# Kernel optimization log

Measured on AMD Instinct MI355X. Metric: run time of the kernel, lower is better.

## Reference

```python
import jax, jax.numpy as jnp
import numpy as np

S, H, R, Z, P = 268, 1024, 8, 8, 4
A = S - Z - P          # actual_hidden_dim = 256
E = min(Z, P)          # min_embed_dim = 4
B = 8192


def setup_inputs() -> dict:
    key = jax.random.key(0)
    ks = jax.random.split(key, 16)
    def g(k, shape, scale=0.02):
        return jax.random.normal(k, shape, dtype=jnp.float32) * scale
    return dict(
        t=jax.random.uniform(ks[0], (1,), dtype=jnp.float32) * 24.0,
        state=jax.random.normal(ks[1], (B, S), dtype=jnp.float32),
        W0=g(ks[2], (H, S + 2)), b0=jnp.zeros((H,), jnp.float32),
        res_W1=g(ks[3], (R, H, H)), res_b1=jnp.zeros((R, H), jnp.float32),
        res_W2=g(ks[4], (R, H, H)), res_b2=jnp.zeros((R, H), jnp.float32),
        Wf=g(ks[5], (S, H)), bf=jnp.zeros((S,), jnp.float32),
        lp_in_w=g(ks[6], (3 * E, E)), lp_in_b=jnp.zeros((3 * E,), jnp.float32),
        lp_out_w=g(ks[7], (E, E)), lp_out_b=jnp.zeros((E,), jnp.float32),
        ta_in_w=g(ks[8], (3 * A, A)), ta_in_b=jnp.zeros((3 * A,), jnp.float32),
        ta_out_w=g(ks[9], (A, A)), ta_out_b=jnp.zeros((A,), jnp.float32),
        loc_proj_w=g(ks[10], (E, Z)), loc_proj_b=jnp.zeros((E,), jnp.float32),
        loc_back_w=g(ks[11], (Z, E)), loc_back_b=jnp.zeros((Z,), jnp.float32),
    )


def reference(t, state, W0, b0, res_W1, res_b1, res_W2, res_b2, Wf, bf,
              lp_in_w, lp_in_b, lp_out_w, lp_out_b,
              ta_in_w, ta_in_b, ta_out_w, ta_out_b,
              loc_proj_w, loc_proj_b, loc_back_w, loc_back_b):
    Bn = state.shape[0]
    # time features: [sin(2*pi*t/24), cos(2*pi*t/24)] broadcast to [B, 2]
    ang = t * (2.0 * jnp.pi / 24.0)
    t_vec = jnp.broadcast_to(jnp.concatenate([jnp.sin(ang), jnp.cos(ang)]), (Bn, 2))

    # core MLP trunk: Linear -> ReLU -> R residual blocks -> Linear
    x = jnp.concatenate([state, t_vec], axis=-1)
    h = jax.nn.relu(x @ W0.T + b0)

    def block(h, p):
        W1, b1, W2, b2 = p
        return jnp.tanh(h + jnp.tanh(h @ W1.T + b1) @ W2.T + b2), None

    h, _ = jax.lax.scan(block, h, (res_W1, res_b1, res_W2, res_b2))
    core = h @ Wf.T + bf  # [B, S]

    # Attention deltas. Both MHA calls have key/value seq_len == 1, so the
    # softmax over a single key is exactly 1.0 and the output reduces exactly
    # to out_proj(v_proj(value)); Q/K projections (and the padded time query)
    # cancel mathematically. Same math as nn.MultiheadAttention here.
    h_part = state[:, :A]
    loc = state[:, A:A + Z]
    loc_p = loc @ loc_proj_w.T + loc_proj_b                   # [B, E]
    v = loc_p @ lp_in_w[2 * E:].T + lp_in_b[2 * E:]           # V projection
    enhanced_loc = v @ lp_out_w.T + lp_out_b                  # out projection
    delta_loc = (enhanced_loc - loc_p) @ loc_back_w.T + loc_back_b  # [B, Z]

    v2 = h_part @ ta_in_w[2 * A:].T + ta_in_b[2 * A:]
    enhanced_h = v2 @ ta_out_w.T + ta_out_b
    delta_h = enhanced_h - h_part                             # [B, A]

    delta = jnp.concatenate(
        [delta_h, delta_loc, jnp.zeros((Bn, P), state.dtype)], axis=-1)
    return core + 0.1 * delta
```

## Files before the change

### kernel.cpp

```cpp
#include <hip/hip_runtime.h>
#include <hip/hip_bf16.h>


typedef unsigned short u16;
typedef __bf16 bf16x8 __attribute__((ext_vector_type(8)));
typedef float f32x4 __attribute__((ext_vector_type(4)));

__device__ __forceinline__ u16 f2b(float f) {
  union { float f; unsigned u; } v; v.f = f;
  unsigned r = v.u + 0x7FFFu + ((v.u >> 16) & 1u);
  return (u16)(r >> 16);
}
__device__ __forceinline__ float b2f(u16 s) {
  union { unsigned u; float f; } v; v.u = ((unsigned)s) << 16;
  return v.f;
}

__device__ __forceinline__ void g2l16(const u16* g, u16* l) {
  __builtin_amdgcn_global_load_lds(
      (__attribute__((address_space(1))) void*)g,
      (__attribute__((address_space(3))) void*)l, 16, 0, 0);
}

template<int MODE, int KK, int LDA>
__global__ __launch_bounds__(512, 2)
void pgemm(const u16* __restrict__ A, const u16* __restrict__ W,
           const float* __restrict__ bias, const u16* __restrict__ resid,
           void* __restrict__ outp, int nreal, int ldo)
{
  extern __shared__ __align__(16) u16 sm[];
  u16* Asb = sm;
  u16* Bsb = sm + 2 * 256 * 64;

  const int tid  = threadIdx.x;
  const int wave = tid >> 6;
  const int lane = tid & 63;
  const int m0 = blockIdx.x << 8;
  const int n0 = blockIdx.y << 7;
  const int wr = wave >> 1, wc = wave & 1;
  const int lrow = lane & 15, quad = lane >> 4;
  const int sw = lrow & 7;

  const int srow  = lane >> 3;
  const int sperm = ((lane & 7) ^ (srow & 7)) << 3;

  const u16* Ag = A + (size_t)(m0 + wave * 32 + srow) * LDA + sperm;
  const u16* Bg = W + (size_t)(n0 + wave * 16 + srow) * KK + sperm;

  f32x4 acc[4][4];
#pragma unroll
  for (int i = 0; i < 4; i++)
#pragma unroll
    for (int j = 0; j < 4; j++) { f32x4 z = {0.f,0.f,0.f,0.f}; acc[i][j] = z; }

#pragma unroll
  for (int g = 0; g < 4; g++)
    g2l16(Ag + (size_t)g * 8 * LDA, Asb + (wave * 32 + g * 8) * 64);
#pragma unroll
  for (int g = 0; g < 2; g++)
    g2l16(Bg + (size_t)g * 8 * KK, Bsb + (wave * 16 + g * 8) * 64);
  __syncthreads();

  const int P = KK / 64;
  for (int p = 0; p < P; p++) {
    if (p + 1 < P) {
      const int ko = (p + 1) << 6;
      const int bo = ((p + 1) & 1);
      u16* aD = Asb + bo * 256 * 64;
      u16* bD = Bsb + bo * 128 * 64;
#pragma unroll
      for (int g = 0; g < 4; g++)
        g2l16(Ag + (size_t)g * 8 * LDA + ko, aD + (wave * 32 + g * 8) * 64);
#pragma unroll
      for (int g = 0; g < 2; g++)
        g2l16(Bg + (size_t)g * 8 * KK + ko, bD + (wave * 16 + g * 8) * 64);
    }
    const u16* aS = Asb + (p & 1) * 256 * 64;
    const u16* bS = Bsb + (p & 1) * 128 * 64;
#pragma unroll
    for (int s = 0; s < 2; s++) {
      const int phys = (s * 4 + quad) ^ sw;
      bf16x8 af[4], bfr[4];
#pragma unroll
      for (int i = 0; i < 4; i++)
        af[i] = *(const bf16x8*)&aS[(wr * 64 + i * 16 + lrow) * 64 + phys * 8];
#pragma unroll
      for (int j = 0; j < 4; j++)
        bfr[j] = *(const bf16x8*)&bS[(wc * 64 + j * 16 + lrow) * 64 + phys * 8];
#pragma unroll
      for (int i = 0; i < 4; i++)
#pragma unroll
        for (int j = 0; j < 4; j++)
          acc[i][j] = __builtin_amdgcn_mfma_f32_16x16x32_bf16(af[i], bfr[j], acc[i][j], 0, 0, 0);
    }
    __syncthreads();
  }

  auto th = [](float x) {
    x = fminf(fmaxf(x, -40.f), 40.f);
    float a = __builtin_amdgcn_exp2f(2.88539008177793f * x);
    return (a - 1.f) * __builtin_amdgcn_rcpf(a + 1.f);
  };

#pragma unroll
  for (int i = 0; i < 4; i++) {
    const int rowb = m0 + wr * 64 + i * 16 + quad * 4;
#pragma unroll
    for (int j = 0; j < 4; j++) {
      const int col = n0 + wc * 64 + j * 16 + lrow;
      const float bi = (col < nreal) ? bias[col] : 0.f;
#pragma unroll
      for (int r = 0; r < 4; r++) {
        const int row = rowb + r;
        float v = acc[i][j][r] + bi;
        if (MODE == 0) {
          v = v > 0.f ? v : 0.f;
          ((u16*)outp)[(size_t)row * ldo + col] = f2b(v);
        } else if (MODE == 1) {
          ((u16*)outp)[(size_t)row * ldo + col] = f2b(th(v));
        } else if (MODE == 2) {
          v += b2f(resid[(size_t)row * ldo + col]);
          ((u16*)outp)[(size_t)row * ldo + col] = f2b(th(v));
        } else if (MODE == 3) {
          if (col < nreal) ((float*)outp)[(size_t)row * ldo + col] = v;
        }
      }
    }
  }
}

__global__ __launch_bounds__(256, 4)
void gemm_bt(const u16* __restrict__ A, const u16* __restrict__ B,
             const float* __restrict__ bias, u16* __restrict__ outp,
             int K, int lda, int ldo)
{
  __shared__ __align__(16) u16 As[64 * 64];
  __shared__ __align__(16) u16 Bs[128 * 64];
  const int tid  = threadIdx.x;
  const int wave = tid >> 6;
  const int lane = tid & 63;
  const int m0 = blockIdx.y << 6;
  const int n0 = blockIdx.x << 7;
  const int wr = wave >> 1, wc = wave & 1;
  const int lrow = lane & 15, quad = lane >> 4;
  const int srow  = lane >> 3;
  const int sperm = ((lane & 7) ^ (srow & 7)) << 3;

  const u16* Ag0 = A + (size_t)(m0 + wave * 16 +  0 + srow) * lda + sperm;
  const u16* Ag1 = A + (size_t)(m0 + wave * 16 +  8 + srow) * lda + sperm;
  const u16* Bg0 = B + (size_t)(n0 + wave * 32 +  0 + srow) * K + sperm;
  const u16* Bg1 = B + (size_t)(n0 + wave * 32 +  8 + srow) * K + sperm;
  const u16* Bg2 = B + (size_t)(n0 + wave * 32 + 16 + srow) * K + sperm;
  const u16* Bg3 = B + (size_t)(n0 + wave * 32 + 24 + srow) * K + sperm;
  u16* Al0 = &As[(wave * 16 +  0) * 64];
  u16* Al1 = &As[(wave * 16 +  8) * 64];
  u16* Bl0 = &Bs[(wave * 32 +  0) * 64];
  u16* Bl1 = &Bs[(wave * 32 +  8) * 64];
  u16* Bl2 = &Bs[(wave * 32 + 16) * 64];
  u16* Bl3 = &Bs[(wave * 32 + 24) * 64];

  f32x4 acc[2][4];
#pragma unroll
  for (int i = 0; i < 2; i++)
#pragma unroll
    for (int j = 0; j < 4; j++) { f32x4 z = {0.f,0.f,0.f,0.f}; acc[i][j] = z; }

  const int swz = lrow & 7;

  for (int k0 = 0; k0 < K; k0 += 64) {
    if (k0) __syncthreads();
    g2l16(Ag0 + k0, Al0);
    g2l16(Ag1 + k0, Al1);
    g2l16(Bg0 + k0, Bl0);
    g2l16(Bg1 + k0, Bl1);
    g2l16(Bg2 + k0, Bl2);
    g2l16(Bg3 + k0, Bl3);
    __syncthreads();
#pragma unroll
    for (int s = 0; s < 2; s++) {
      const int c = (s * 4 + quad) ^ swz;
      bf16x8 af[2], bfr[4];
#pragma unroll
      for (int i = 0; i < 2; i++)
        af[i] = *(const bf16x8*)&As[(wr * 32 + i * 16 + lrow) * 64 + c * 8];
#pragma unroll
      for (int j = 0; j < 4; j++)
        bfr[j] = *(const bf16x8*)&Bs[(wc * 64 + j * 16 + lrow) * 64 + c * 8];
#pragma unroll
      for (int i = 0; i < 2; i++)
#pragma unroll
        for (int j = 0; j < 4; j++)
          acc[i][j] = __builtin_amdgcn_mfma_f32_16x16x32_bf16(af[i], bfr[j], acc[i][j], 0, 0, 0);
    }
  }

#pragma unroll
  for (int i = 0; i < 2; i++) {
    const int rowb = m0 + wr * 32 + i * 16 + quad * 4;
#pragma unroll
    for (int j = 0; j < 4; j++) {
      const int col = n0 + wc * 64 + j * 16 + lrow;
      const float bi = bias[col];
#pragma unroll
      for (int r = 0; r < 4; r++)
        outp[(size_t)(rowb + r) * ldo + col] = f2b(acc[i][j][r] + bi);
    }
  }
}

__global__ void conv_bulk(const float* __restrict__ w1, const float* __restrict__ w2,
                          u16* __restrict__ o1, u16* __restrict__ o2)
{
  const int n4 = (8 * 1024 * 1024) / 4;
  int i = blockIdx.x * 256 + threadIdx.x;
  const float* src; u16* dst;
  if (i < n4) { src = w1; dst = o1; }
  else        { i -= n4; if (i >= n4) return; src = w2; dst = o2; }
  float4 v = ((const float4*)src)[i];
  unsigned p0 = (unsigned)f2b(v.x) | ((unsigned)f2b(v.y) << 16);
  unsigned p1 = (unsigned)f2b(v.z) | ((unsigned)f2b(v.w) << 16);
  uint2 pk; pk.x = p0; pk.y = p1;
  ((uint2*)dst)[i] = pk;
}

__global__ void conv_misc(const float* __restrict__ W0, const float* __restrict__ Wf,
                          const float* __restrict__ ta_in_w, const float* __restrict__ ta_out_w,
                          const float* __restrict__ state, const float* __restrict__ t,
                          u16* __restrict__ w0_bf, u16* __restrict__ wf_bf,
                          u16* __restrict__ taA, u16* __restrict__ taB,
                          u16* __restrict__ x_bf)
{
  int i = blockIdx.x * 256 + threadIdx.x;
  const int nW0 = 1024 * 384;
  const int nWf = 384 * 1024;
  const int nTa = 256 * 256;
  const int nX  = 8192 * 384;
  if (i < nW0) {
    int o = i / 384, k = i - o * 384;
    w0_bf[i] = (k < 270) ? f2b(W0[o * 270 + k]) : (u16)0;
    return;
  }
  i -= nW0;
  if (i < nWf) {
    int n = i >> 10;
    wf_bf[i] = (n < 268) ? f2b(Wf[i]) : (u16)0;
    return;
  }
  i -= nWf;
  if (i < nTa) { taA[i] = f2b(ta_in_w[512 * 256 + i]); return; }
  i -= nTa;
  if (i < nTa) { taB[i] = f2b(ta_out_w[i]); return; }
  i -= nTa;
  if (i < nX) {
    int r = i / 384, c = i - r * 384;
    u16 v;
    if (c < 268) v = f2b(state[r * 268 + c]);
    else if (c == 268) { float ang = t[0] * 0.2617993877991494f; v = f2b(sinf(ang)); }
    else if (c == 269) { float ang = t[0] * 0.2617993877991494f; v = f2b(cosf(ang)); }
    else v = 0;
    x_bf[i] = v;
  }
}

__global__ void add_delta(float* __restrict__ out, const u16* __restrict__ eh,
                          const float* __restrict__ state,
                          const float* __restrict__ lp_in_w, const float* __restrict__ lp_in_b,
                          const float* __restrict__ lp_out_w, const float* __restrict__ lp_out_b,
                          const float* __restrict__ loc_proj_w, const float* __restrict__ loc_proj_b,
                          const float* __restrict__ loc_back_w, const float* __restrict__ loc_back_b)
{
  const int idx = blockIdx.x * 256 + threadIdx.x;
  if (idx >= 8192 * 268) return;
  const int row = idx / 268;
  const int col = idx - row * 268;
  if (col < 256) {
    out[idx] += 0.1f * (b2f(eh[row * 256 + col]) - state[idx]);
  } else if (col < 264) {
    const float* srow = state + row * 268 + 256;
    float locp[4], vv[4], dd[4];
#pragma unroll
    for (int e = 0; e < 4; e++) {
      float s = loc_proj_b[e];
#pragma unroll
      for (int z = 0; z < 8; z++) s += loc_proj_w[e * 8 + z] * srow[z];
      locp[e] = s;
    }
#pragma unroll
    for (int e = 0; e < 4; e++) {
      float s = lp_in_b[8 + e];
#pragma unroll
      for (int j = 0; j < 4; j++) s += lp_in_w[(8 + e) * 4 + j] * locp[j];
      vv[e] = s;
    }
#pragma unroll
    for (int e = 0; e < 4; e++) {
      float s = lp_out_b[e];
#pragma unroll
      for (int j = 0; j < 4; j++) s += lp_out_w[e * 4 + j] * vv[j];
      dd[e] = s - locp[e];
    }
    const int z = col - 256;
    float s = loc_back_b[z];
#pragma unroll
    for (int e = 0; e < 4; e++) s += loc_back_w[z * 4 + e] * dd[e];
    out[idx] += 0.1f * s;
  }
}

extern "C" void kernel_launch(void* const* d_in, const int* in_sizes, int n_in,
                              void* d_out, int out_size, void* d_ws, size_t ws_size,
                              hipStream_t stream)
{
  const float* t          = (const float*)d_in[0];
  const float* state      = (const float*)d_in[1];
  const float* W0         = (const float*)d_in[2];
  const float* b0         = (const float*)d_in[3];
  const float* rW1        = (const float*)d_in[4];
  const float* rb1        = (const float*)d_in[5];
  const float* rW2        = (const float*)d_in[6];
  const float* rb2        = (const float*)d_in[7];
  const float* Wf         = (const float*)d_in[8];
  const float* bfv        = (const float*)d_in[9];
  const float* lp_in_w    = (const float*)d_in[10];
  const float* lp_in_b    = (const float*)d_in[11];
  const float* lp_out_w   = (const float*)d_in[12];
  const float* lp_out_b   = (const float*)d_in[13];
  const float* ta_in_w    = (const float*)d_in[14];
  const float* ta_in_b    = (const float*)d_in[15];
  const float* ta_out_w   = (const float*)d_in[16];
  const float* ta_out_b   = (const float*)d_in[17];
  const float* loc_proj_w = (const float*)d_in[18];
  const float* loc_proj_b = (const float*)d_in[19];
  const float* loc_back_w = (const float*)d_in[20];
  const float* loc_back_b = (const float*)d_in[21];
  float* out = (float*)d_out;

  char* ws = (char*)d_ws;
  auto alloc = [&](size_t bytes) { char* p = ws; ws += (bytes + 255) & ~(size_t)255; return p; };
  u16* rw1_bf = (u16*)alloc((size_t)8 * 1024 * 1024 * 2);
  u16* rw2_bf = (u16*)alloc((size_t)8 * 1024 * 1024 * 2);
  u16* w0_bf  = (u16*)alloc((size_t)1024 * 384 * 2);
  u16* wf_bf  = (u16*)alloc((size_t)384 * 1024 * 2);
  u16* taA_bf = (u16*)alloc((size_t)256 * 256 * 2);
  u16* taB_bf = (u16*)alloc((size_t)256 * 256 * 2);
  u16* x_bf   = (u16*)alloc((size_t)8192 * 384 * 2);
  u16* h_bf   = (u16*)alloc((size_t)8192 * 1024 * 2);
  u16* tmp_bf = (u16*)alloc((size_t)8192 * 1024 * 2);
  u16* v2_bf  = (u16*)alloc((size_t)8192 * 256 * 2);
  u16* eh_bf  = (u16*)alloc((size_t)8192 * 256 * 2);

  const int lds = (2 * 256 * 64 + 2 * 128 * 64) * 2;
  hipFuncSetAttribute(reinterpret_cast<const void*>(pgemm<0, 384, 384>),
                      hipFuncAttributeMaxDynamicSharedMemorySize, lds);
  hipFuncSetAttribute(reinterpret_cast<const void*>(pgemm<1, 1024, 1024>),
                      hipFuncAttributeMaxDynamicSharedMemorySize, lds);
  hipFuncSetAttribute(reinterpret_cast<const void*>(pgemm<2, 1024, 1024>),
                      hipFuncAttributeMaxDynamicSharedMemorySize, lds);
  hipFuncSetAttribute(reinterpret_cast<const void*>(pgemm<3, 1024, 1024>),
                      hipFuncAttributeMaxDynamicSharedMemorySize, lds);

  conv_bulk<<<16384, 256, 0, stream>>>(rW1, rW2, rw1_bf, rw2_bf);
  conv_misc<<<15872, 256, 0, stream>>>(W0, Wf, ta_in_w, ta_out_w, state, t,
                                       w0_bf, wf_bf, taA_bf, taB_bf, x_bf);

  pgemm<0, 384, 384><<<dim3(32, 8), 512, lds, stream>>>(x_bf, w0_bf, b0, nullptr, h_bf, 1024, 1024);

  for (int r = 0; r < 8; r++) {
    pgemm<1, 1024, 1024><<<dim3(32, 8), 512, lds, stream>>>(
        h_bf, rw1_bf + ((size_t)r << 20), rb1 + (r << 10), nullptr, tmp_bf, 1024, 1024);
    pgemm<2, 1024, 1024><<<dim3(32, 8), 512, lds, stream>>>(
        tmp_bf, rw2_bf + ((size_t)r << 20), rb2 + (r << 10), h_bf, h_bf, 1024, 1024);
  }

  gemm_bt<<<dim3(2, 128), 256, 0, stream>>>(x_bf, taA_bf, ta_in_b + 512, v2_bf, 256, 384, 256);
  gemm_bt<<<dim3(2, 128), 256, 0, stream>>>(v2_bf, taB_bf, ta_out_b, eh_bf, 256, 256, 256);

  pgemm<3, 1024, 1024><<<dim3(32, 3), 512, lds, stream>>>(h_bf, wf_bf, bfv, nullptr, out, 268, 268);

  add_delta<<<8576, 256, 0, stream>>>(out, eh_bf, state,
                                      lp_in_w, lp_in_b, lp_out_w, lp_out_b,
                                      loc_proj_w, loc_proj_b, loc_back_w, loc_back_b);
}
```

Before: 582.1 us.

## Triple-buffer GEMM LDS pipeline with vmcnt-based waits and MFMA priority

Replaces the two-stage LDS double buffer in the bf16 GEMM with a three-stage ring that prefetches two K-tiles ahead. The full __syncthreads per iteration becomes explicit vmcnt waits plus a raw s_barrier, and MFMA sections are wrapped in s_setprio. The goal is to hide global-to-LDS latency better. In exchange LDS per block grows from 96KB to 144KB, which likely cuts resident blocks per CU from two to one.

```diff
diff --git a/kernel.cpp b/kernel.cpp
--- a/kernel.cpp
+++ b/kernel.cpp
@@ -29,8 +29,7 @@
            void* __restrict__ outp, int nreal, int ldo)
 {
   extern __shared__ __align__(16) u16 sm[];
-  u16* Asb = sm;
-  u16* Bsb = sm + 2 * 256 * 64;
+  constexpr int BUFSZ = (256 + 128) * 64;
 
   const int tid  = threadIdx.x;
   const int wave = tid >> 6;
@@ -53,30 +52,34 @@
 #pragma unroll
     for (int j = 0; j < 4; j++) { f32x4 z = {0.f,0.f,0.f,0.f}; acc[i][j] = z; }
 
-#pragma unroll
-  for (int g = 0; g < 4; g++)
-    g2l16(Ag + (size_t)g * 8 * LDA, Asb + (wave * 32 + g * 8) * 64);
-#pragma unroll
-  for (int g = 0; g < 2; g++)
-    g2l16(Bg + (size_t)g * 8 * KK, Bsb + (wave * 16 + g * 8) * 64);
-  __syncthreads();
-
-  const int P = KK / 64;
-  for (int p = 0; p < P; p++) {
-    if (p + 1 < P) {
-      const int ko = (p + 1) << 6;
-      const int bo = ((p + 1) & 1);
-      u16* aD = Asb + bo * 256 * 64;
-      u16* bD = Bsb + bo * 128 * 64;
-#pragma unroll
-      for (int g = 0; g < 4; g++)
-        g2l16(Ag + (size_t)g * 8 * LDA + ko, aD + (wave * 32 + g * 8) * 64);
-#pragma unroll
-      for (int g = 0; g < 2; g++)
-        g2l16(Bg + (size_t)g * 8 * KK + ko, bD + (wave * 16 + g * 8) * 64);
-    }
-    const u16* aS = Asb + (p & 1) * 256 * 64;
-    const u16* bS = Bsb + (p & 1) * 128 * 64;
+  auto stage = [&](int p, int buf) {
+    const int ko = p << 6;
+    u16* aD = sm + buf * BUFSZ;
+    u16* bD = aD + 256 * 64;
+#pragma unroll
+    for (int g = 0; g < 4; g++)
+      g2l16(Ag + (size_t)g * 8 * LDA + ko, aD + (wave * 32 + g * 8) * 64);
+#pragma unroll
+    for (int g = 0; g < 2; g++)
+      g2l16(Bg + (size_t)g * 8 * KK + ko, bD + (wave * 16 + g * 8) * 64);
+  };
+
+  constexpr int P = KK / 64;
+
+  stage(0, 0);
+  stage(1, 1);
+  asm volatile("s_waitcnt vmcnt(6)" ::: "memory");
+  __builtin_amdgcn_s_barrier();
+  __builtin_amdgcn_sched_barrier(0);
+
+#pragma unroll
+  for (int p = 0; p < P; ++p) {
+    const int cur = p % 3;
+    const int stg = (p + 2) % 3;
+    if (p + 2 < P) stage(p + 2, stg);
+
+    const u16* aS = sm + cur * BUFSZ;
+    const u16* bS = aS + 256 * 64;
 #pragma unroll
     for (int s = 0; s < 2; s++) {
       const int phys = (s * 4 + quad) ^ sw;
@@ -87,13 +90,23 @@
 #pragma unroll
       for (int j = 0; j < 4; j++)
         bfr[j] = *(const bf16x8*)&bS[(wc * 64 + j * 16 + lrow) * 64 + phys * 8];
+      __builtin_amdgcn_s_setprio(1);
 #pragma unroll
       for (int i = 0; i < 4; i++)
 #pragma unroll
         for (int j = 0; j < 4; j++)
           acc[i][j] = __builtin_amdgcn_mfma_f32_16x16x32_bf16(af[i], bfr[j], acc[i][j], 0, 0, 0);
-    }
-    __syncthreads();
+      __builtin_amdgcn_s_setprio(0);
+    }
+
+    if (p + 1 < P) {
+      __builtin_amdgcn_sched_barrier(0);
+      if (p + 2 < P) { asm volatile("s_waitcnt vmcnt(6)" ::: "memory"); }
+      else           { asm volatile("s_waitcnt vmcnt(0)" ::: "memory"); }
+      __builtin_amdgcn_sched_barrier(0);
+      __builtin_amdgcn_s_barrier();
+      __builtin_amdgcn_sched_barrier(0);
+    }
   }
 
   auto th = [](float x) {
@@ -349,7 +362,7 @@
   u16* v2_bf  = (u16*)alloc((size_t)8192 * 256 * 2);
   u16* eh_bf  = (u16*)alloc((size_t)8192 * 256 * 2);
 
-  const int lds = (2 * 256 * 64 + 2 * 128 * 64) * 2;
+  const int lds = 3 * (256 + 128) * 64 * 2;
   hipFuncSetAttribute(reinterpret_cast<const void*>(pgemm<0, 384, 384>),
                       hipFuncAttributeMaxDynamicSharedMemorySize, lds);
   hipFuncSetAttribute(reinterpret_cast<const void*>(pgemm<1, 1024, 1024>),
```

Result: no change. 591.2 us (+1.6%).

## Shrink pgemm tile to 128x128 with 256 threads and drop double buffering

Applied to the files above, without the earlier changes.

Changes the main GEMM kernel from a 256x128 tile with 512 threads and double-buffered dynamic LDS to a 128x128 tile with 256 threads and a single static LDS buffer. The grid doubles along M, giving 512 blocks per GEMM instead of 256, which spreads work more evenly across the GPU's compute units. The cost is that loads are no longer overlapped with MFMA work, since each step waits for its own load. Each block also reuses less data, so more traffic goes through L2.

```diff
diff --git a/kernel.cpp b/kernel.cpp
--- a/kernel.cpp
+++ b/kernel.cpp
@@ -23,19 +23,18 @@
 }
 
 template<int MODE, int KK, int LDA>
-__global__ __launch_bounds__(512, 2)
+__global__ __launch_bounds__(256, 3)
 void pgemm(const u16* __restrict__ A, const u16* __restrict__ W,
            const float* __restrict__ bias, const u16* __restrict__ resid,
            void* __restrict__ outp, int nreal, int ldo)
 {
-  extern __shared__ __align__(16) u16 sm[];
-  u16* Asb = sm;
-  u16* Bsb = sm + 2 * 256 * 64;
+  __shared__ __align__(16) u16 As[128 * 64];
+  __shared__ __align__(16) u16 Bs[128 * 64];
 
   const int tid  = threadIdx.x;
   const int wave = tid >> 6;
   const int lane = tid & 63;
-  const int m0 = blockIdx.x << 8;
+  const int m0 = blockIdx.x << 7;
   const int n0 = blockIdx.y << 7;
   const int wr = wave >> 1, wc = wave & 1;
   const int lrow = lane & 15, quad = lane >> 4;
@@ -45,7 +44,7 @@
   const int sperm = ((lane & 7) ^ (srow & 7)) << 3;
 
   const u16* Ag = A + (size_t)(m0 + wave * 32 + srow) * LDA + sperm;
-  const u16* Bg = W + (size_t)(n0 + wave * 16 + srow) * KK + sperm;
+  const u16* Bg = W + (size_t)(n0 + wave * 32 + srow) * KK + sperm;
 
   f32x4 acc[4][4];
 #pragma unroll
@@ -53,47 +52,35 @@
 #pragma unroll
     for (int j = 0; j < 4; j++) { f32x4 z = {0.f,0.f,0.f,0.f}; acc[i][j] = z; }
 
-#pragma unroll
-  for (int g = 0; g < 4; g++)
-    g2l16(Ag + (size_t)g * 8 * LDA, Asb + (wave * 32 + g * 8) * 64);
-#pragma unroll
-  for (int g = 0; g < 2; g++)
-    g2l16(Bg + (size_t)g * 8 * KK, Bsb + (wave * 16 + g * 8) * 64);
-  __syncthreads();
-
-  const int P = KK / 64;
-  for (int p = 0; p < P; p++) {
-    if (p + 1 < P) {
-      const int ko = (p + 1) << 6;
-      const int bo = ((p + 1) & 1);
-      u16* aD = Asb + bo * 256 * 64;
-      u16* bD = Bsb + bo * 128 * 64;
-#pragma unroll
-      for (int g = 0; g < 4; g++)
-        g2l16(Ag + (size_t)g * 8 * LDA + ko, aD + (wave * 32 + g * 8) * 64);
-#pragma unroll
-      for (int g = 0; g < 2; g++)
-        g2l16(Bg + (size_t)g * 8 * KK + ko, bD + (wave * 16 + g * 8) * 64);
-    }
-    const u16* aS = Asb + (p & 1) * 256 * 64;
-    const u16* bS = Bsb + (p & 1) * 128 * 64;
+  constexpr int P = KK / 64;
+
+  for (int p = 0; p < P; ++p) {
+    const int ko = p << 6;
+    if (p) __syncthreads();
+#pragma unroll
+    for (int g = 0; g < 4; g++)
+      g2l16(Ag + (size_t)g * 8 * LDA + ko, &As[(wave * 32 + g * 8) * 64]);
+#pragma unroll
+    for (int g = 0; g < 4; g++)
+      g2l16(Bg + (size_t)g * 8 * KK + ko, &Bs[(wave * 32 + g * 8) * 64]);
+    __syncthreads();
+
 #pragma unroll
     for (int s = 0; s < 2; s++) {
       const int phys = (s * 4 + quad) ^ sw;
       bf16x8 af[4], bfr[4];
 #pragma unroll
       for (int i = 0; i < 4; i++)
-        af[i] = *(const bf16x8*)&aS[(wr * 64 + i * 16 + lrow) * 64 + phys * 8];
+        af[i] = *(const bf16x8*)&As[(wr * 64 + i * 16 + lrow) * 64 + phys * 8];
 #pragma unroll
       for (int j = 0; j < 4; j++)
-        bfr[j] = *(const bf16x8*)&bS[(wc * 64 + j * 16 + lrow) * 64 + phys * 8];
+        bfr[j] = *(const bf16x8*)&Bs[(wc * 64 + j * 16 + lrow) * 64 + phys * 8];
 #pragma unroll
       for (int i = 0; i < 4; i++)
 #pragma unroll
         for (int j = 0; j < 4; j++)
           acc[i][j] = __builtin_amdgcn_mfma_f32_16x16x32_bf16(af[i], bfr[j], acc[i][j], 0, 0, 0);
     }
-    __syncthreads();
   }
 
   auto th = [](float x) {
@@ -349,33 +336,23 @@
   u16* v2_bf  = (u16*)alloc((size_t)8192 * 256 * 2);
   u16* eh_bf  = (u16*)alloc((size_t)8192 * 256 * 2);
 
-  const int lds = (2 * 256 * 64 + 2 * 128 * 64) * 2;
-  hipFuncSetAttribute(reinterpret_cast<const void*>(pgemm<0, 384, 384>),
-                      hipFuncAttributeMaxDynamicSharedMemorySize, lds);
-  hipFuncSetAttribute(reinterpret_cast<const void*>(pgemm<1, 1024, 1024>),
-                      hipFuncAttributeMaxDynamicSharedMemorySize, lds);
-  hipFuncSetAttribute(reinterpret_cast<const void*>(pgemm<2, 1024, 1024>),
-                      hipFuncAttributeMaxDynamicSharedMemorySize, lds);
-  hipFuncSetAttribute(reinterpret_cast<const void*>(pgemm<3, 1024, 1024>),
-                      hipFuncAttributeMaxDynamicSharedMemorySize, lds);
-
   conv_bulk<<<16384, 256, 0, stream>>>(rW1, rW2, rw1_bf, rw2_bf);
   conv_misc<<<15872, 256, 0, stream>>>(W0, Wf, ta_in_w, ta_out_w, state, t,
                                        w0_bf, wf_bf, taA_bf, taB_bf, x_bf);
 
-  pgemm<0, 384, 384><<<dim3(32, 8), 512, lds, stream>>>(x_bf, w0_bf, b0, nullptr, h_bf, 1024, 1024);
+  pgemm<0, 384, 384><<<dim3(64, 8), 256, 0, stream>>>(x_bf, w0_bf, b0, nullptr, h_bf, 1024, 1024);
 
   for (int r = 0; r < 8; r++) {
-    pgemm<1, 1024, 1024><<<dim3(32, 8), 512, lds, stream>>>(
+    pgemm<1, 1024, 1024><<<dim3(64, 8), 256, 0, stream>>>(
         h_bf, rw1_bf + ((size_t)r << 20), rb1 + (r << 10), nullptr, tmp_bf, 1024, 1024);
-    pgemm<2, 1024, 1024><<<dim3(32, 8), 512, lds, stream>>>(
+    pgemm<2, 1024, 1024><<<dim3(64, 8), 256, 0, stream>>>(
         tmp_bf, rw2_bf + ((size_t)r << 20), rb2 + (r << 10), h_bf, h_bf, 1024, 1024);
   }
 
   gemm_bt<<<dim3(2, 128), 256, 0, stream>>>(x_bf, taA_bf, ta_in_b + 512, v2_bf, 256, 384, 256);
   gemm_bt<<<dim3(2, 128), 256, 0, stream>>>(v2_bf, taB_bf, ta_out_b, eh_bf, 256, 256, 256);
 
-  pgemm<3, 1024, 1024><<<dim3(32, 3), 512, lds, stream>>>(h_bf, wf_bf, bfv, nullptr, out, 268, 268);
+  pgemm<3, 1024, 1024><<<dim3(64, 3), 256, 0, stream>>>(h_bf, wf_bf, bfv, nullptr, out, 268, 268);
 
   add_delta<<<8576, 256, 0, stream>>>(out, eh_bf, state,
                                       lp_in_w, lp_in_b, lp_out_w, lp_out_b,
```

Result: slower. 612.9 us (+5.3%).
